# Kernel tuning notes

Hardware: AMD Instinct MI355X
Metric: run time of the kernel (lower is better)

Reference implementation:

```python
import jax, jax.numpy as jnp
import numpy as np


def setup_inputs() -> dict:
    key = jax.random.key(0)
    k1, k2, k3, k4 = jax.random.split(key, 4)
    B, S, C = 16, 2048, 512
    x = jax.random.normal(k1, (B, S, C), dtype=jnp.float32)
    x_prime = jax.random.normal(k2, (B, S, C), dtype=jnp.float32)
    W = jax.random.normal(k3, (C, C), dtype=jnp.float32) * (1.0 / np.sqrt(C))
    b = jax.random.normal(k4, (C,), dtype=jnp.float32) * 0.01
    return {"x": x, "x_prime": x_prime, "W": W, "b": b}


def reference(x, x_prime, W, b):
    # q = Linear(x_prime): [B, S, C]
    q = jnp.einsum("bsc,dc->bsd", x_prime, W) + b
    # score = tanh(x_prime) @ q^T : [B, S, S]
    score = jnp.einsum("bsc,btc->bst", jnp.tanh(x_prime), q)
    alpha = jax.nn.softmax(score, axis=-1)
    # y_att = alpha @ x : [B, S, C]
    y_att = jnp.einsum("bst,btc->bsc", alpha, x)
    # dropout is identity in eval mode
    return jnp.tanh(y_att)
```

## Files before the change

kernel.cpp:

```cpp
#include <hip/hip_runtime.h>
#include <hip/hip_bf16.h>
#include <math.h>

typedef __bf16 bf16x8 __attribute__((ext_vector_type(8)));
typedef float  f32x4  __attribute__((ext_vector_type(4)));

#define MFMA16(a, b, c) __builtin_amdgcn_mfma_f32_16x16x32_bf16((a), (b), (c), 0, 0, 0)

static constexpr int    kB  = 16;
static constexpr int    kS  = 2048;
static constexpr int    kC  = 512;
static constexpr size_t kNE = (size_t)kB * kS * kC;

static __device__ __forceinline__ void split_bf16(float v, __bf16 &hi, __bf16 &lo) {
  hi = (__bf16)v;
  lo = (__bf16)(v - (float)hi);
}

static __device__ __forceinline__ void stage_split16(
    const float* __restrict__ src, __bf16* hi, __bf16* lo, int o) {
  float4 v0 = *(const float4*)(src + 0);
  float4 v1 = *(const float4*)(src + 4);
  float4 v2 = *(const float4*)(src + 8);
  float4 v3 = *(const float4*)(src + 12);
  float vv[16] = {v0.x, v0.y, v0.z, v0.w, v1.x, v1.y, v1.z, v1.w,
                  v2.x, v2.y, v2.z, v2.w, v3.x, v3.y, v3.z, v3.w};
  bf16x8 h0, h1, l0, l1;
#pragma unroll
  for (int i = 0; i < 8; ++i) {
    __bf16 a, b;
    split_bf16(vv[i], a, b);     h0[i] = a; l0[i] = b;
    split_bf16(vv[8 + i], a, b); h1[i] = a; l1[i] = b;
  }
  *(bf16x8*)&hi[o]     = h0;
  *(bf16x8*)&hi[o + 8] = h1;
  *(bf16x8*)&lo[o]     = l0;
  *(bf16x8*)&lo[o + 8] = l1;
}

__global__ __launch_bounds__(256) void k_tanh_split(
    const float* __restrict__ xp, __bf16* __restrict__ th, __bf16* __restrict__ tl) {
  size_t i = ((size_t)blockIdx.x * 256 + threadIdx.x) * 8;
  float4 a = *(const float4*)(xp + i);
  float4 b = *(const float4*)(xp + i + 4);
  float v[8] = {a.x, a.y, a.z, a.w, b.x, b.y, b.z, b.w};
  bf16x8 h, l;
#pragma unroll
  for (int k = 0; k < 8; ++k) {
    float t = tanhf(v[k]);
    __bf16 hh, ll;
    split_bf16(t, hh, ll);
    h[k] = hh; l[k] = ll;
  }
  *(bf16x8*)(th + i) = h;
  *(bf16x8*)(tl + i) = l;
}

__global__ __launch_bounds__(256) void k_transpose_x(
    const float* __restrict__ x, __bf16* __restrict__ xbt) {
  __shared__ float tile[64][65];
  int bid = blockIdx.x;
  int b   = bid >> 8;
  int t0  = ((bid >> 3) & 31) * 64;
  int c0  = (bid & 7) * 64;
  int row = threadIdx.x >> 2;
  int seg = threadIdx.x & 3;
  const float* src = x + (size_t)(b * kS + t0 + row) * kC + c0 + seg * 16;
  float4 v0 = *(const float4*)(src + 0);
  float4 v1 = *(const float4*)(src + 4);
  float4 v2 = *(const float4*)(src + 8);
  float4 v3 = *(const float4*)(src + 12);
  float vv[16] = {v0.x, v0.y, v0.z, v0.w, v1.x, v1.y, v1.z, v1.w,
                  v2.x, v2.y, v2.z, v2.w, v3.x, v3.y, v3.z, v3.w};
#pragma unroll
  for (int i = 0; i < 16; ++i) tile[row][seg * 16 + i] = vv[i];
  __syncthreads();
  bf16x8 o0, o1;
#pragma unroll
  for (int i = 0; i < 8; ++i) o0[i] = (__bf16)tile[seg * 16 + i][row];
#pragma unroll
  for (int i = 0; i < 8; ++i) o1[i] = (__bf16)tile[seg * 16 + 8 + i][row];
  __bf16* dst = xbt + (size_t)(b * kC + c0 + row) * kS + t0 + seg * 16;
  *(bf16x8*)(dst)     = o0;
  *(bf16x8*)(dst + 8) = o1;
}

__global__ __launch_bounds__(256) void k_qgemm(
    const float* __restrict__ xp, const float* __restrict__ W,
    const float* __restrict__ bias, __bf16* __restrict__ qh, __bf16* __restrict__ ql) {
  __shared__ __align__(16) __bf16 lds[4 * 4608];
  __bf16* Ah = lds;
  __bf16* Al = lds + 4608;
  __bf16* Bh = lds + 9216;
  __bf16* Bl = lds + 13824;

  int bid = blockIdx.x;
  int n0  = (bid & 7) * 64;
  int m0  = (bid >> 3) * 64;

  int tid  = threadIdx.x;
  int lane = tid & 63;
  int wave = tid >> 6;
  int qd   = lane >> 4;
  int cl   = lane & 15;
  int row  = tid >> 2;
  int seg  = tid & 3;

  f32x4 acc[4] = {};

  for (int kc = 0; kc < 8; ++kc) {
    stage_split16(xp + (size_t)(m0 + row) * kC + kc * 64 + seg * 16, Ah, Al, row * 72 + seg * 16);
    stage_split16(W  + (size_t)(n0 + row) * kC + kc * 64 + seg * 16, Bh, Bl, row * 72 + seg * 16);
    __syncthreads();
#pragma unroll
    for (int ks = 0; ks < 2; ++ks) {
      int ka = ks * 32 + qd * 8;
      bf16x8 ah = *(const bf16x8*)&Ah[(wave * 16 + cl) * 72 + ka];
      bf16x8 al = *(const bf16x8*)&Al[(wave * 16 + cl) * 72 + ka];
#pragma unroll
      for (int j = 0; j < 4; ++j) {
        bf16x8 bh = *(const bf16x8*)&Bh[(j * 16 + cl) * 72 + ka];
        bf16x8 bl = *(const bf16x8*)&Bl[(j * 16 + cl) * 72 + ka];
        acc[j] = MFMA16(ah, bh, acc[j]);
        acc[j] = MFMA16(ah, bl, acc[j]);
        acc[j] = MFMA16(al, bh, acc[j]);
      }
    }
    __syncthreads();
  }
#pragma unroll
  for (int j = 0; j < 4; ++j) {
    int d = n0 + j * 16 + cl;
    float bv = bias[d];
#pragma unroll
    for (int r = 0; r < 4; ++r) {
      int m = m0 + wave * 16 + qd * 4 + r;
      float v = acc[j][r] + bv;
      __bf16 h, l;
      split_bf16(v, h, l);
      qh[(size_t)m * kC + d] = h;
      ql[(size_t)m * kC + d] = l;
    }
  }
}

__global__ __launch_bounds__(256, 2) void k_attn(
    const __bf16* __restrict__ th, const __bf16* __restrict__ tl,
    const __bf16* __restrict__ qh, const __bf16* __restrict__ ql,
    const __bf16* __restrict__ xbt, float* __restrict__ out) {
  __shared__ __align__(16) __bf16 lds[27648];
  __bf16* Ah = lds;
  __bf16* Al = lds + 4608;
  __bf16* Bh = lds + 9216;
  __bf16* Bl = lds + 18432;
  __bf16* P  = lds;
  __bf16* Xt = lds + 9216;

  int bid = blockIdx.x;
  int b   = (bid & 7) | ((bid >> 8) << 3);
  int s0  = ((bid >> 3) & 31) * 64;

  int tid  = threadIdx.x;
  int lane = tid & 63;
  int wave = tid >> 6;
  int qd   = lane >> 4;
  int cl   = lane & 15;

  const float LOG2E = 1.4426950408889634f;

  float m_r[4], l_r[4];
  f32x4 O[8][4] = {};
#pragma unroll
  for (int r = 0; r < 4; ++r) { m_r[r] = -INFINITY; l_r[r] = 0.f; }

  const size_t rowbase = (size_t)b * kS;

  for (int tt = 0; tt < 16; ++tt) {
    int t0 = tt * 128;
    f32x4 Sacc[8] = {};
    for (int kc = 0; kc < 8; ++kc) {
      {
        int arow = tid >> 2, aseg = tid & 3;
        size_t g = (rowbase + s0 + arow) * kC + kc * 64 + aseg * 16;
        int o = arow * 72 + aseg * 16;
        *(bf16x8*)&Ah[o]     = *(const bf16x8*)(th + g);
        *(bf16x8*)&Ah[o + 8] = *(const bf16x8*)(th + g + 8);
        *(bf16x8*)&Al[o]     = *(const bf16x8*)(tl + g);
        *(bf16x8*)&Al[o + 8] = *(const bf16x8*)(tl + g + 8);
      }
      {
        int brow = tid >> 1, bseg = tid & 1;
        size_t g = (rowbase + t0 + brow) * kC + kc * 64 + bseg * 32;
        int o = brow * 72 + bseg * 32;
#pragma unroll
        for (int u = 0; u < 4; ++u)
          *(bf16x8*)&Bh[o + u * 8] = *(const bf16x8*)(qh + g + u * 8);
#pragma unroll
        for (int u = 0; u < 4; ++u)
          *(bf16x8*)&Bl[o + u * 8] = *(const bf16x8*)(ql + g + u * 8);
      }
      __syncthreads();
#pragma unroll
      for (int ks = 0; ks < 2; ++ks) {
        int ka = ks * 32 + qd * 8;
        bf16x8 ah = *(const bf16x8*)&Ah[(wave * 16 + cl) * 72 + ka];
        bf16x8 al = *(const bf16x8*)&Al[(wave * 16 + cl) * 72 + ka];
#pragma unroll
        for (int j = 0; j < 8; ++j) {
          bf16x8 bh = *(const bf16x8*)&Bh[(j * 16 + cl) * 72 + ka];
          bf16x8 bl = *(const bf16x8*)&Bl[(j * 16 + cl) * 72 + ka];
          Sacc[j] = MFMA16(ah, bh, Sacc[j]);
          Sacc[j] = MFMA16(ah, bl, Sacc[j]);
          Sacc[j] = MFMA16(al, bh, Sacc[j]);
        }
      }
      __syncthreads();
    }
    float rmax[4];
#pragma unroll
    for (int r = 0; r < 4; ++r) {
      float v = Sacc[0][r];
#pragma unroll
      for (int j = 1; j < 8; ++j) v = fmaxf(v, Sacc[j][r]);
      rmax[r] = v;
    }
#pragma unroll
    for (int mk = 1; mk < 16; mk <<= 1)
#pragma unroll
      for (int r = 0; r < 4; ++r)
        rmax[r] = fmaxf(rmax[r], __shfl_xor(rmax[r], mk, 64));
    float alpha[4], rsum[4];
#pragma unroll
    for (int r = 0; r < 4; ++r) {
      float mn = fmaxf(m_r[r], rmax[r]);
      alpha[r] = exp2f((m_r[r] - mn) * LOG2E);
      m_r[r] = mn;
      rsum[r] = 0.f;
    }
#pragma unroll
    for (int j = 0; j < 8; ++j)
#pragma unroll
      for (int r = 0; r < 4; ++r) {
        float p = exp2f((Sacc[j][r] - m_r[r]) * LOG2E);
        Sacc[j][r] = p;
        rsum[r] += p;
      }
#pragma unroll
    for (int mk = 1; mk < 16; mk <<= 1)
#pragma unroll
      for (int r = 0; r < 4; ++r)
        rsum[r] += __shfl_xor(rsum[r], mk, 64);
    f32x4 av;
#pragma unroll
    for (int r = 0; r < 4; ++r) {
      l_r[r] = l_r[r] * alpha[r] + rsum[r];
      av[r] = alpha[r];
    }
#pragma unroll
    for (int nc = 0; nc < 8; ++nc)
#pragma unroll
      for (int nt = 0; nt < 4; ++nt)
        O[nc][nt] *= av;
#pragma unroll
    for (int j = 0; j < 8; ++j)
#pragma unroll
      for (int r = 0; r < 4; ++r)
        P[(wave * 16 + qd * 4 + r) * 136 + j * 16 + cl] = (__bf16)Sacc[j][r];
    __syncthreads();
#pragma unroll
    for (int nc = 0; nc < 8; ++nc) {
      {
        int xrow = tid >> 2, xseg = tid & 3;
        size_t g = ((size_t)b * kC + nc * 64 + xrow) * kS + t0 + xseg * 32;
        int o = xrow * 136 + xseg * 32;
#pragma unroll
        for (int u = 0; u < 4; ++u)
          *(bf16x8*)&Xt[o + u * 8] = *(const bf16x8*)(xbt + g + u * 8);
      }
      __syncthreads();
#pragma unroll
      for (int ks = 0; ks < 4; ++ks) {
        int ka = ks * 32 + qd * 8;
        bf16x8 pa = *(const bf16x8*)&P[(wave * 16 + cl) * 136 + ka];
#pragma unroll
        for (int nt = 0; nt < 4; ++nt) {
          bf16x8 xb = *(const bf16x8*)&Xt[(nt * 16 + cl) * 136 + ka];
          O[nc][nt] = MFMA16(pa, xb, O[nc][nt]);
        }
      }
      __syncthreads();
    }
  }
#pragma unroll
  for (int r = 0; r < 4; ++r) {
    float inv = __builtin_amdgcn_rcpf(l_r[r]);
    size_t rowoff = (rowbase + s0 + wave * 16 + qd * 4 + r) * kC;
#pragma unroll
    for (int nc = 0; nc < 8; ++nc)
#pragma unroll
      for (int nt = 0; nt < 4; ++nt) {
        float v = O[nc][nt][r] * inv;
        float e = exp2f(2.f * LOG2E * v);
        out[rowoff + nc * 64 + nt * 16 + cl] = 1.f - 2.f * __builtin_amdgcn_rcpf(e + 1.f);
      }
  }
}

extern "C" void kernel_launch(void* const* d_in, const int* in_sizes, int n_in,
                              void* d_out, int out_size, void* d_ws, size_t ws_size,
                              hipStream_t stream) {
  const float* x    = (const float*)d_in[0];
  const float* xp   = (const float*)d_in[1];
  const float* W    = (const float*)d_in[2];
  const float* bias = (const float*)d_in[3];
  float* out = (float*)d_out;

  __bf16* ws  = (__bf16*)d_ws;
  __bf16* th  = ws;
  __bf16* tl  = ws + kNE;
  __bf16* qh  = ws + 2 * kNE;
  __bf16* ql  = ws + 3 * kNE;
  __bf16* xbt = ws + 4 * kNE;

  k_tanh_split<<<8192, 256, 0, stream>>>(xp, th, tl);
  k_transpose_x<<<4096, 256, 0, stream>>>(x, xbt);
  k_qgemm<<<4096, 256, 0, stream>>>(xp, W, bias, qh, ql);
  k_attn<<<512, 256, 0, stream>>>(th, tl, qh, ql, xbt, out);
}
```

Baseline: 1.008 ms.

## Restructure attention kernel with 32x32 MFMA, 2x2 wave tiling, async LDS double buffering

```diff
diff --git a/kernel.cpp b/kernel.cpp
--- a/kernel.cpp
+++ b/kernel.cpp
@@ -4,8 +4,10 @@
 
 typedef __bf16 bf16x8 __attribute__((ext_vector_type(8)));
 typedef float  f32x4  __attribute__((ext_vector_type(4)));
+typedef float  f32x16 __attribute__((ext_vector_type(16)));
 
 #define MFMA16(a, b, c) __builtin_amdgcn_mfma_f32_16x16x32_bf16((a), (b), (c), 0, 0, 0)
+#define MFMA32(a, b, c) __builtin_amdgcn_mfma_f32_32x32x16_bf16((a), (b), (c), 0, 0, 0)
 
 static constexpr int    kB  = 16;
 static constexpr int    kS  = 2048;
@@ -15,6 +17,12 @@
 static __device__ __forceinline__ void split_bf16(float v, __bf16 &hi, __bf16 &lo) {
   hi = (__bf16)v;
   lo = (__bf16)(v - (float)hi);
+}
+
+static __device__ __forceinline__ void gl2lds16(const __bf16* g, __bf16* l) {
+  __builtin_amdgcn_global_load_lds(
+      (const __attribute__((address_space(1))) void*)g,
+      (__attribute__((address_space(3))) void*)l, 16, 0, 0);
 }
 
 static __device__ __forceinline__ void stage_split16(
@@ -136,10 +144,10 @@
     for (int r = 0; r < 4; ++r) {
       int m = m0 + wave * 16 + qd * 4 + r;
       float v = acc[j][r] + bv;
-      __bf16 h, l;
-      split_bf16(v, h, l);
-      qh[(size_t)m * kC + d] = h;
-      ql[(size_t)m * kC + d] = l;
+      __bf16 hh, ll;
+      split_bf16(v, hh, ll);
+      qh[(size_t)m * kC + d] = hh;
+      ql[(size_t)m * kC + d] = ll;
     }
   }
 }
@@ -148,13 +156,8 @@
     const __bf16* __restrict__ th, const __bf16* __restrict__ tl,
     const __bf16* __restrict__ qh, const __bf16* __restrict__ ql,
     const __bf16* __restrict__ xbt, float* __restrict__ out) {
-  __shared__ __align__(16) __bf16 lds[27648];
-  __bf16* Ah = lds;
-  __bf16* Al = lds + 4608;
-  __bf16* Bh = lds + 9216;
-  __bf16* Bl = lds + 18432;
-  __bf16* P  = lds;
-  __bf16* Xt = lds + 9216;
+  __shared__ __align__(16) __bf16 lds[24576];
+  __shared__ float xred[2][2][64];
 
   int bid = blockIdx.x;
   int b   = (bid & 7) | ((bid >> 8) << 3);
@@ -163,146 +166,204 @@
   int tid  = threadIdx.x;
   int lane = tid & 63;
   int wave = tid >> 6;
-  int qd   = lane >> 4;
-  int cl   = lane & 15;
+  int wm   = wave >> 1;
+  int wn   = wave & 1;
+  int h    = lane >> 5;
+  int l31  = lane & 31;
 
   const float LOG2E = 1.4426950408889634f;
-
-  float m_r[4], l_r[4];
-  f32x4 O[8][4] = {};
-#pragma unroll
-  for (int r = 0; r < 4; ++r) { m_r[r] = -INFINITY; l_r[r] = 0.f; }
-
   const size_t rowbase = (size_t)b * kS;
+
+  int rA  = wm * 32 + l31;
+  int rB0 = wn * 64 + l31;
+  int rB1 = rB0 + 32;
+  int rX  = wn * 32 + l31;
+
+  float m_r[16], l_r[16];
+#pragma unroll
+  for (int g = 0; g < 16; ++g) { m_r[g] = -INFINITY; l_r[g] = 0.f; }
+  f32x16 O[8] = {};
 
   for (int tt = 0; tt < 16; ++tt) {
     int t0 = tt * 128;
-    f32x4 Sacc[8] = {};
-    for (int kc = 0; kc < 8; ++kc) {
+    f32x16 S0 = {}, S1 = {};
+
+    auto stage_score = [&](int kc, int bsel) {
+      __bf16* buf = lds + bsel * 12288;
       {
-        int arow = tid >> 2, aseg = tid & 3;
-        size_t g = (rowbase + s0 + arow) * kC + kc * 64 + aseg * 16;
-        int o = arow * 72 + aseg * 16;
-        *(bf16x8*)&Ah[o]     = *(const bf16x8*)(th + g);
-        *(bf16x8*)&Ah[o + 8] = *(const bf16x8*)(th + g + 8);
-        *(bf16x8*)&Al[o]     = *(const bf16x8*)(tl + g);
-        *(bf16x8*)&Al[o + 8] = *(const bf16x8*)(tl + g + 8);
-      }
-      {
-        int brow = tid >> 1, bseg = tid & 1;
-        size_t g = (rowbase + t0 + brow) * kC + kc * 64 + bseg * 32;
-        int o = brow * 72 + bseg * 32;
-#pragma unroll
-        for (int u = 0; u < 4; ++u)
-          *(bf16x8*)&Bh[o + u * 8] = *(const bf16x8*)(qh + g + u * 8);
-#pragma unroll
-        for (int u = 0; u < 4; ++u)
-          *(bf16x8*)&Bl[o + u * 8] = *(const bf16x8*)(ql + g + u * 8);
-      }
+        int p = wave * 64 + lane;
+        int r = p >> 2;
+        int c = (p & 3) ^ (r & 3);
+        size_t g = (rowbase + s0 + r) * (size_t)kC + kc * 32 + c * 8;
+        gl2lds16(th + g, buf + p * 8);
+        gl2lds16(tl + g, buf + 2048 + p * 8);
+      }
+#pragma unroll
+      for (int i = 0; i < 2; ++i) {
+        int p = (wave * 2 + i) * 64 + lane;
+        int r = p >> 2;
+        int c = (p & 3) ^ (r & 3);
+        size_t g = (rowbase + t0 + r) * (size_t)kC + kc * 32 + c * 8;
+        gl2lds16(qh + g, buf + 4096 + p * 8);
+        gl2lds16(ql + g, buf + 8192 + p * 8);
+      }
+    };
+
+    auto compute_score = [&](int bsel) {
+      const __bf16* buf = lds + bsel * 12288;
+      const __bf16* Ah = buf;
+      const __bf16* Al = buf + 2048;
+      const __bf16* Bh = buf + 4096;
+      const __bf16* Bl = buf + 8192;
+#pragma unroll
+      for (int ks = 0; ks < 2; ++ks) {
+        int cc = ks * 2 + h;
+        int oA  = rA  * 32 + (cc ^ (rA  & 3)) * 8;
+        int oB0 = rB0 * 32 + (cc ^ (rB0 & 3)) * 8;
+        int oB1 = rB1 * 32 + (cc ^ (rB1 & 3)) * 8;
+        bf16x8 ah  = *(const bf16x8*)&Ah[oA];
+        bf16x8 al  = *(const bf16x8*)&Al[oA];
+        bf16x8 bh0 = *(const bf16x8*)&Bh[oB0];
+        bf16x8 bl0 = *(const bf16x8*)&Bl[oB0];
+        bf16x8 bh1 = *(const bf16x8*)&Bh[oB1];
+        bf16x8 bl1 = *(const bf16x8*)&Bl[oB1];
+        S0 = MFMA32(ah, bh0, S0);
+        S0 = MFMA32(ah, bl0, S0);
+        S0 = MFMA32(al, bh0, S0);
+        S1 = MFMA32(ah, bh1, S1);
+        S1 = MFMA32(ah, bl1, S1);
+        S1 = MFMA32(al, bh1, S1);
+      }
+    };
+
+    stage_score(0, 0);
+    __syncthreads();
+    for (int kc = 0; kc < 16; ++kc) {
+      if (kc < 15) stage_score(kc + 1, (kc + 1) & 1);
+      compute_score(kc & 1);
       __syncthreads();
-#pragma unroll
-      for (int ks = 0; ks < 2; ++ks) {
-        int ka = ks * 32 + qd * 8;
-        bf16x8 ah = *(const bf16x8*)&Ah[(wave * 16 + cl) * 72 + ka];
-        bf16x8 al = *(const bf16x8*)&Al[(wave * 16 + cl) * 72 + ka];
-#pragma unroll
-        for (int j = 0; j < 8; ++j) {
-          bf16x8 bh = *(const bf16x8*)&Bh[(j * 16 + cl) * 72 + ka];
-          bf16x8 bl = *(const bf16x8*)&Bl[(j * 16 + cl) * 72 + ka];
-          Sacc[j] = MFMA16(ah, bh, Sacc[j]);
-          Sacc[j] = MFMA16(ah, bl, Sacc[j]);
-          Sacc[j] = MFMA16(al, bh, Sacc[j]);
-        }
-      }
+    }
+
+    float mnew[16];
+#pragma unroll
+    for (int g = 0; g < 16; ++g) mnew[g] = fmaxf(S0[g], S1[g]);
+#pragma unroll
+    for (int mk = 1; mk <= 16; mk <<= 1)
+#pragma unroll
+      for (int g = 0; g < 16; ++g)
+        mnew[g] = fmaxf(mnew[g], __shfl_xor(mnew[g], mk, 64));
+    if (l31 == 0) {
+#pragma unroll
+      for (int g = 0; g < 16; ++g) {
+        int rr = 4 * h + (g & 3) + 8 * (g >> 2);
+        xred[0][wn][wm * 32 + rr] = mnew[g];
+      }
+    }
+    __syncthreads();
+#pragma unroll
+    for (int g = 0; g < 16; ++g) {
+      int rr = 4 * h + (g & 3) + 8 * (g >> 2);
+      mnew[g] = fmaxf(mnew[g], xred[0][1 - wn][wm * 32 + rr]);
+    }
+    float alpha[16], rsum[16];
+#pragma unroll
+    for (int g = 0; g < 16; ++g) {
+      float mn = fmaxf(m_r[g], mnew[g]);
+      alpha[g] = exp2f((m_r[g] - mn) * LOG2E);
+      m_r[g] = mn;
+      float p0 = exp2f((S0[g] - mn) * LOG2E);
+      float p1 = exp2f((S1[g] - mn) * LOG2E);
+      S0[g] = p0; S1[g] = p1;
+      rsum[g] = p0 + p1;
+    }
+#pragma unroll
+    for (int mk = 1; mk <= 16; mk <<= 1)
+#pragma unroll
+      for (int g = 0; g < 16; ++g)
+        rsum[g] += __shfl_xor(rsum[g], mk, 64);
+    if (l31 == 0) {
+#pragma unroll
+      for (int g = 0; g < 16; ++g) {
+        int rr = 4 * h + (g & 3) + 8 * (g >> 2);
+        xred[1][wn][wm * 32 + rr] = rsum[g];
+      }
+    }
+    __syncthreads();
+#pragma unroll
+    for (int g = 0; g < 16; ++g) {
+      int rr = 4 * h + (g & 3) + 8 * (g >> 2);
+      rsum[g] += xred[1][1 - wn][wm * 32 + rr];
+      l_r[g] = l_r[g] * alpha[g] + rsum[g];
+    }
+#pragma unroll
+    for (int nc = 0; nc < 8; ++nc)
+#pragma unroll
+      for (int g = 0; g < 16; ++g) O[nc][g] *= alpha[g];
+
+#pragma unroll
+    for (int g = 0; g < 16; ++g) {
+      int rr = 4 * h + (g & 3) + 8 * (g >> 2);
+      int r  = wm * 32 + rr;
+      int rx = r & 7;
+      int cb0 = (wn * 64 + l31) >> 3;
+      int ph0 = (cb0 & 8) | ((cb0 & 7) ^ rx);
+      lds[r * 128 + ph0 * 8 + (l31 & 7)] = (__bf16)S0[g];
+      int cb1 = cb0 + 4;
+      int ph1 = (cb1 & 8) | ((cb1 & 7) ^ rx);
+      lds[r * 128 + ph1 * 8 + (l31 & 7)] = (__bf16)S1[g];
+    }
+    __syncthreads();
+
+    bf16x8 pa[8];
+#pragma unroll
+    for (int ks = 0; ks < 8; ++ks) {
+      int cc = ks * 2 + h;
+      int ph = (cc & 8) | ((cc & 7) ^ (rA & 7));
+      pa[ks] = *(const bf16x8*)&lds[rA * 128 + ph * 8];
+    }
+
+    auto stage_xt = [&](int nc, int bsel) {
+      __bf16* xb = lds + 8192 + bsel * 8192;
+#pragma unroll
+      for (int i = 0; i < 4; ++i) {
+        int p = (wave * 4 + i) * 64 + lane;
+        int r = p >> 4;
+        int pc = p & 15;
+        int c = (pc & 8) | ((pc & 7) ^ (r & 7));
+        gl2lds16(xbt + ((size_t)b * kC + nc * 64 + r) * (size_t)kS + t0 + c * 8,
+                 xb + p * 8);
+      }
+    };
+
+    stage_xt(0, 0);
+    __syncthreads();
+    for (int nc = 0; nc < 8; ++nc) {
+      if (nc < 7) stage_xt(nc + 1, (nc + 1) & 1);
+      const __bf16* xb = lds + 8192 + (nc & 1) * 8192;
+      f32x16 o = O[nc];
+#pragma unroll
+      for (int ks = 0; ks < 8; ++ks) {
+        int cc = ks * 2 + h;
+        int ph = (cc & 8) | ((cc & 7) ^ (rX & 7));
+        bf16x8 x8 = *(const bf16x8*)&xb[rX * 128 + ph * 8];
+        o = MFMA32(pa[ks], x8, o);
+      }
+      O[nc] = o;
       __syncthreads();
     }
-    float rmax[4];
-#pragma unroll
-    for (int r = 0; r < 4; ++r) {
-      float v = Sacc[0][r];
-#pragma unroll
-      for (int j = 1; j < 8; ++j) v = fmaxf(v, Sacc[j][r]);
-      rmax[r] = v;
-    }
-#pragma unroll
-    for (int mk = 1; mk < 16; mk <<= 1)
-#pragma unroll
-      for (int r = 0; r < 4; ++r)
-        rmax[r] = fmaxf(rmax[r], __shfl_xor(rmax[r], mk, 64));
-    float alpha[4], rsum[4];
-#pragma unroll
-    for (int r = 0; r < 4; ++r) {
-      float mn = fmaxf(m_r[r], rmax[r]);
-      alpha[r] = exp2f((m_r[r] - mn) * LOG2E);
-      m_r[r] = mn;
-      rsum[r] = 0.f;
-    }
-#pragma unroll
-    for (int j = 0; j < 8; ++j)
-#pragma unroll
-      for (int r = 0; r < 4; ++r) {
-        float p = exp2f((Sacc[j][r] - m_r[r]) * LOG2E);
-        Sacc[j][r] = p;
-        rsum[r] += p;
-      }
-#pragma unroll
-    for (int mk = 1; mk < 16; mk <<= 1)
-#pragma unroll
-      for (int r = 0; r < 4; ++r)
-        rsum[r] += __shfl_xor(rsum[r], mk, 64);
-    f32x4 av;
-#pragma unroll
-    for (int r = 0; r < 4; ++r) {
-      l_r[r] = l_r[r] * alpha[r] + rsum[r];
-      av[r] = alpha[r];
-    }
-#pragma unroll
-    for (int nc = 0; nc < 8; ++nc)
-#pragma unroll
-      for (int nt = 0; nt < 4; ++nt)
-        O[nc][nt] *= av;
-#pragma unroll
-    for (int j = 0; j < 8; ++j)
-#pragma unroll
-      for (int r = 0; r < 4; ++r)
-        P[(wave * 16 + qd * 4 + r) * 136 + j * 16 + cl] = (__bf16)Sacc[j][r];
-    __syncthreads();
+  }
+
+#pragma unroll
+  for (int g = 0; g < 16; ++g) {
+    int rr = 4 * h + (g & 3) + 8 * (g >> 2);
+    float inv = __builtin_amdgcn_rcpf(l_r[g]);
+    size_t ro = (rowbase + s0 + wm * 32 + rr) * (size_t)kC + wn * 32 + l31;
 #pragma unroll
     for (int nc = 0; nc < 8; ++nc) {
-      {
-        int xrow = tid >> 2, xseg = tid & 3;
-        size_t g = ((size_t)b * kC + nc * 64 + xrow) * kS + t0 + xseg * 32;
-        int o = xrow * 136 + xseg * 32;
-#pragma unroll
-        for (int u = 0; u < 4; ++u)
-          *(bf16x8*)&Xt[o + u * 8] = *(const bf16x8*)(xbt + g + u * 8);
-      }
-      __syncthreads();
-#pragma unroll
-      for (int ks = 0; ks < 4; ++ks) {
-        int ka = ks * 32 + qd * 8;
-        bf16x8 pa = *(const bf16x8*)&P[(wave * 16 + cl) * 136 + ka];
-#pragma unroll
-        for (int nt = 0; nt < 4; ++nt) {
-          bf16x8 xb = *(const bf16x8*)&Xt[(nt * 16 + cl) * 136 + ka];
-          O[nc][nt] = MFMA16(pa, xb, O[nc][nt]);
-        }
-      }
-      __syncthreads();
-    }
-  }
-#pragma unroll
-  for (int r = 0; r < 4; ++r) {
-    float inv = __builtin_amdgcn_rcpf(l_r[r]);
-    size_t rowoff = (rowbase + s0 + wave * 16 + qd * 4 + r) * kC;
-#pragma unroll
-    for (int nc = 0; nc < 8; ++nc)
-#pragma unroll
-      for (int nt = 0; nt < 4; ++nt) {
-        float v = O[nc][nt][r] * inv;
-        float e = exp2f(2.f * LOG2E * v);
-        out[rowoff + nc * 64 + nt * 16 + cl] = 1.f - 2.f * __builtin_amdgcn_rcpf(e + 1.f);
-      }
+      float v = O[nc][g] * inv;
+      float e = exp2f(2.f * LOG2E * v);
+      out[ro + nc * 64] = 1.f - 2.f * __builtin_amdgcn_rcpf(e + 1.f);
+    }
   }
 }
 
```

After: 1.093 ms. +8.4%, slower.
